# Optimization experiments

Measured on AMD Instinct MI355X. Metric: run time of the kernel, lower is better.

## Reference

```python
import jax, jax.numpy as jnp
import numpy as np

H = 4      # heads
DK = 64    # d // heads
EPS = 1e-5 # LayerNorm eps

def setup_inputs() -> dict:
    key = jax.random.key(0)
    ks = jax.random.split(key, 8)
    N, NC, D = 16384, 32, 256
    s = 0.02
    return {
        'parent_vec': jax.random.normal(ks[0], (N, D), jnp.float32),
        'child_vecs': jax.random.normal(ks[1], (N, NC, D), jnp.float32),
        'child_idx': jax.random.randint(ks[2], (N, NC), 0, NC, jnp.int64),
        'Wq': jax.random.normal(ks[3], (D, D), jnp.float32) * s,
        'Wkv': jax.random.normal(ks[4], (2 * D, D), jnp.float32) * s,
        'pos_emb': jax.random.normal(ks[5], (NC, D), jnp.float32) * s,
        'Wout': jax.random.normal(ks[6], (D, D), jnp.float32) * s,
        'bout': jnp.zeros((D,), jnp.float32),
        'ln_gamma': jnp.ones((D,), jnp.float32),
        'ln_beta': jnp.zeros((D,), jnp.float32),
    }

def reference(parent_vec, child_vecs, child_idx, Wq, Wkv, pos_emb, Wout, bout, ln_gamma, ln_beta):
    N, NC, D = child_vecs.shape
    # add position embedding to each child (gather)
    kv_in = child_vecs + pos_emb[child_idx]                     # [N, NC, D]
    kv = jnp.einsum('bnd,ed->bne', kv_in, Wkv)                  # [N, NC, 2D]
    k, v = jnp.split(kv, 2, axis=-1)
    k = k.reshape(N, NC, H, DK)
    v = v.reshape(N, NC, H, DK)
    q = (parent_vec @ Wq.T).reshape(N, H, DK)                   # [N, H, DK]
    scores = jnp.einsum('bnhd,bhd->bnh', k, q) * (DK ** -0.5)   # [N, NC, H]
    att = jax.nn.softmax(scores, axis=1)                        # over children
    ctx = jnp.einsum('bnh,bnhd->bhd', att, v).reshape(N, D)     # [N, D]
    out = ctx @ Wout.T + bout                                   # dropout: eval mode (identity)
    x = parent_vec + out
    mu = jnp.mean(x, axis=-1, keepdims=True)
    var = jnp.var(x, axis=-1, keepdims=True)
    return (x - mu) * jax.lax.rsqrt(var + EPS) * ln_gamma + ln_beta
```

## Files before the change

### kernel.cpp

```cpp
#include <hip/hip_runtime.h>
#include <hip/hip_bf16.h>
#include <string.h>

typedef __attribute__((ext_vector_type(8))) short short8;
typedef __attribute__((ext_vector_type(4))) float f32x4;

#define D_DIM 256
#define NC_DIM 32
#define KV_PAD 260

__device__ __forceinline__ ushort f2bf(float x) {
    union { float f; unsigned u; } v; v.f = x;
    unsigned r = (v.u + 0x7fffu + ((v.u >> 16) & 1u)) >> 16;
    return (ushort)r;
}
__device__ __forceinline__ float bf2f(ushort u) {
    union { unsigned u32; float f; } v; v.u32 = ((unsigned)u) << 16;
    return v.f;
}

__global__ __launch_bounds__(256)
void k_combine_B(const float* __restrict__ Wq, const float* __restrict__ Wkv,
                 ushort* __restrict__ Bc2t) {
    int bid = blockIdx.x;
    int h = bid >> 8, d = bid & 255;
    int i = threadIdx.x;
    __shared__ float wk_s[64];
    if (i < 64) wk_s[i] = Wkv[(size_t)(h * 64 + i) * D_DIM + d];
    __syncthreads();
    float s = 0.f;
#pragma unroll 8
    for (int j = 0; j < 64; j++)
        s = fmaf(Wq[(size_t)(h * 64 + j) * D_DIM + i], wk_s[j], s);
    Bc2t[(size_t)(h * 256 + d) * D_DIM + i] = f2bf(s);
}

__global__ __launch_bounds__(256)
void k_combine_C(const float* __restrict__ Wkv, const float* __restrict__ Wout,
                 ushort* __restrict__ Cc2t) {
    int bid = blockIdx.x;
    int h = bid >> 8, i = bid & 255;
    int d = threadIdx.x;
    __shared__ float wo_s[64];
    if (d < 64) wo_s[d] = Wout[(size_t)i * D_DIM + h * 64 + d];
    __syncthreads();
    const float* Wv = Wkv + 256 * D_DIM;
    float s = 0.f;
#pragma unroll 8
    for (int dk = 0; dk < 64; dk++)
        s = fmaf(Wv[(size_t)(h * 64 + dk) * D_DIM + d], wo_s[dk], s);
    Cc2t[(size_t)i * 1024 + h * 256 + d] = f2bf(s);
}

template <bool A_F32, bool EPI_RES>
__global__ __launch_bounds__(256)
void k_gemm(const void* __restrict__ Ap, const ushort* __restrict__ Bt,
            void* __restrict__ Cp, const float* __restrict__ resid,
            const float* __restrict__ bias, int M, int N, int K) {
    __shared__ ushort As[64][40];
    __shared__ ushort Bs[64][40];
    const int tid = threadIdx.x;
    const int m0 = blockIdx.y * 64, n0 = blockIdx.x * 64;
    const int w = tid >> 6, L = tid & 63;
    const int ar = tid >> 2, ac = (tid & 3) * 8;
    f32x4 acc0 = {0.f, 0.f, 0.f, 0.f}, acc1 = {0.f, 0.f, 0.f, 0.f};
    f32x4 acc2 = {0.f, 0.f, 0.f, 0.f}, acc3 = {0.f, 0.f, 0.f, 0.f};

    for (int k0 = 0; k0 < K; k0 += 32) {
        __syncthreads();
        if (A_F32) {
            const float* A = (const float*)Ap;
            const float* src = A + (size_t)(m0 + ar) * K + k0 + ac;
            float4 v0 = *(const float4*)src;
            float4 v1 = *(const float4*)(src + 4);
            union { ushort us[8]; uint4 v; } pk;
            pk.us[0] = f2bf(v0.x); pk.us[1] = f2bf(v0.y);
            pk.us[2] = f2bf(v0.z); pk.us[3] = f2bf(v0.w);
            pk.us[4] = f2bf(v1.x); pk.us[5] = f2bf(v1.y);
            pk.us[6] = f2bf(v1.z); pk.us[7] = f2bf(v1.w);
            *(uint4*)&As[ar][ac] = pk.v;
        } else {
            const ushort* A = (const ushort*)Ap;
            *(uint4*)&As[ar][ac] = *(const uint4*)(A + (size_t)(m0 + ar) * K + k0 + ac);
        }
        *(uint4*)&Bs[ar][ac] = *(const uint4*)(Bt + (size_t)(n0 + ar) * K + k0 + ac);
        __syncthreads();
        short8 af = *(const short8*)&As[w * 16 + (L & 15)][(L >> 4) * 8];
        short8 b0 = *(const short8*)&Bs[0 + (L & 15)][(L >> 4) * 8];
        short8 b1 = *(const short8*)&Bs[16 + (L & 15)][(L >> 4) * 8];
        short8 b2 = *(const short8*)&Bs[32 + (L & 15)][(L >> 4) * 8];
        short8 b3 = *(const short8*)&Bs[48 + (L & 15)][(L >> 4) * 8];
        acc0 = __builtin_amdgcn_mfma_f32_16x16x32_bf16(af, b0, acc0, 0, 0, 0);
        acc1 = __builtin_amdgcn_mfma_f32_16x16x32_bf16(af, b1, acc1, 0, 0, 0);
        acc2 = __builtin_amdgcn_mfma_f32_16x16x32_bf16(af, b2, acc2, 0, 0, 0);
        acc3 = __builtin_amdgcn_mfma_f32_16x16x32_bf16(af, b3, acc3, 0, 0, 0);
    }
    const int row_base = m0 + w * 16 + (L >> 4) * 4;
    const int col_base = n0 + (L & 15);
    f32x4 accs[4] = {acc0, acc1, acc2, acc3};
#pragma unroll
    for (int nt = 0; nt < 4; nt++) {
        int col = col_base + nt * 16;
#pragma unroll
        for (int r = 0; r < 4; r++) {
            int row = row_base + r;
            float v = accs[nt][r];
            if (EPI_RES) {
                ((float*)Cp)[(size_t)row * N + col] =
                    v + resid[(size_t)row * N + col] + bias[col];
            } else {
                ((ushort*)Cp)[(size_t)row * N + col] = f2bf(v);
            }
        }
    }
}

__global__ __launch_bounds__(256)
void k_attn(const float* __restrict__ child, const int* __restrict__ idx,
            const float* __restrict__ pos_emb, ushort* __restrict__ Am) {
    __shared__ int idx_s[NC_DIM];
    __shared__ float A_s[4][KV_PAD];
    __shared__ float kv_s[NC_DIM][KV_PAD];
    __shared__ float part_s[8][NC_DIM][4];
    __shared__ float att_s[NC_DIM][4];
    __shared__ float mpart_s[4][4][D_DIM];
    const int b = blockIdx.x;
    const int t = threadIdx.x;

    if (t < NC_DIM) idx_s[t] = idx[(size_t)b * NC_DIM + t];
    if (t < 128) {
        uint4 raw = *(const uint4*)(Am + (size_t)b * 1024 + t * 8);
        const ushort* u = (const ushort*)&raw;
        int h = t >> 5, c = (t & 31) * 8;
#pragma unroll
        for (int j = 0; j < 8; j++) A_s[h][c + j] = bf2f(u[j]);
    }
    __syncthreads();

    const float4* ch4 = (const float4*)(child + (size_t)b * NC_DIM * D_DIM);
#pragma unroll
    for (int i = 0; i < 8; i++) {
        int f = t + i * 256;
        int n = f >> 6, c4 = f & 63;
        float4 cv = ch4[f];
        float4 pv = ((const float4*)(pos_emb + (size_t)idx_s[n] * D_DIM))[c4];
        float4 r;
        r.x = cv.x + pv.x; r.y = cv.y + pv.y; r.z = cv.z + pv.z; r.w = cv.w + pv.w;
        *(float4*)&kv_s[n][c4 * 4] = r;
    }
    __syncthreads();

    {
        int n = t & 31, c = t >> 5;
        float s0 = 0, s1 = 0, s2 = 0, s3 = 0;
#pragma unroll
        for (int j = 0; j < 32; j += 4) {
            float4 kv = *(const float4*)&kv_s[n][c * 32 + j];
            float4 a0 = *(const float4*)&A_s[0][c * 32 + j];
            float4 a1 = *(const float4*)&A_s[1][c * 32 + j];
            float4 a2 = *(const float4*)&A_s[2][c * 32 + j];
            float4 a3 = *(const float4*)&A_s[3][c * 32 + j];
            s0 += kv.x * a0.x + kv.y * a0.y + kv.z * a0.z + kv.w * a0.w;
            s1 += kv.x * a1.x + kv.y * a1.y + kv.z * a1.z + kv.w * a1.w;
            s2 += kv.x * a2.x + kv.y * a2.y + kv.z * a2.z + kv.w * a2.w;
            s3 += kv.x * a3.x + kv.y * a3.y + kv.z * a3.z + kv.w * a3.w;
        }
        part_s[c][n][0] = s0; part_s[c][n][1] = s1;
        part_s[c][n][2] = s2; part_s[c][n][3] = s3;
    }
    __syncthreads();

    if (t < 128) {
        int n = t & 31, h = t >> 5;
        float s = 0;
#pragma unroll
        for (int c = 0; c < 8; c++) s += part_s[c][n][h];
        s *= 0.125f;
        float mx = s;
#pragma unroll
        for (int off = 16; off; off >>= 1) mx = fmaxf(mx, __shfl_xor(mx, off, 32));
        float e = __expf(s - mx);
        float sum = e;
#pragma unroll
        for (int off = 16; off; off >>= 1) sum += __shfl_xor(sum, off, 32);
        att_s[n][h] = e / sum;
    }
    __syncthreads();

    {
        int d4 = t & 63, g = t >> 6;
        float4 a0 = {0, 0, 0, 0}, a1 = {0, 0, 0, 0}, a2 = {0, 0, 0, 0}, a3 = {0, 0, 0, 0};
#pragma unroll
        for (int nn = 0; nn < 8; nn++) {
            int n = g * 8 + nn;
            float4 kv = *(const float4*)&kv_s[n][d4 * 4];
            float w0 = att_s[n][0], w1 = att_s[n][1], w2 = att_s[n][2], w3 = att_s[n][3];
            a0.x += w0 * kv.x; a0.y += w0 * kv.y; a0.z += w0 * kv.z; a0.w += w0 * kv.w;
            a1.x += w1 * kv.x; a1.y += w1 * kv.y; a1.z += w1 * kv.z; a1.w += w1 * kv.w;
            a2.x += w2 * kv.x; a2.y += w2 * kv.y; a2.z += w2 * kv.z; a2.w += w2 * kv.w;
            a3.x += w3 * kv.x; a3.y += w3 * kv.y; a3.z += w3 * kv.z; a3.w += w3 * kv.w;
        }
        *(float4*)&mpart_s[g][0][d4 * 4] = a0;
        *(float4*)&mpart_s[g][1][d4 * 4] = a1;
        *(float4*)&mpart_s[g][2][d4 * 4] = a2;
        *(float4*)&mpart_s[g][3][d4 * 4] = a3;
    }
    __syncthreads();

    {
        int h = t >> 6, d4 = t & 63;
        float4 m = {0, 0, 0, 0};
#pragma unroll
        for (int g = 0; g < 4; g++) {
            float4 p = *(const float4*)&mpart_s[g][h][d4 * 4];
            m.x += p.x; m.y += p.y; m.z += p.z; m.w += p.w;
        }
        union { ushort us[4]; uint2 v; } pk;
        pk.us[0] = f2bf(m.x); pk.us[1] = f2bf(m.y);
        pk.us[2] = f2bf(m.z); pk.us[3] = f2bf(m.w);
        *(uint2*)(Am + (size_t)b * 1024 + h * 256 + d4 * 4) = pk.v;
    }
}

__global__ __launch_bounds__(256)
void k_ln(const float* __restrict__ x, const float* __restrict__ gamma,
          const float* __restrict__ beta, float* __restrict__ out) {
    const int t = threadIdx.x;
    const int w = t >> 6, l = t & 63;
    const size_t row = (size_t)blockIdx.x * 4 + w;
    float4 v = *(const float4*)(x + row * D_DIM + l * 4);
    float s = v.x + v.y + v.z + v.w;
    float q = v.x * v.x + v.y * v.y + v.z * v.z + v.w * v.w;
#pragma unroll
    for (int off = 32; off; off >>= 1) {
        s += __shfl_xor(s, off, 64);
        q += __shfl_xor(q, off, 64);
    }
    float mu = s * (1.f / 256.f);
    float var = q * (1.f / 256.f) - mu * mu;
    float rs = rsqrtf(var + 1e-5f);
    float4 g4 = *(const float4*)(gamma + l * 4);
    float4 b4 = *(const float4*)(beta + l * 4);
    float4 o;
    o.x = (v.x - mu) * rs * g4.x + b4.x;
    o.y = (v.y - mu) * rs * g4.y + b4.y;
    o.z = (v.z - mu) * rs * g4.z + b4.z;
    o.w = (v.w - mu) * rs * g4.w + b4.w;
    *(float4*)(out + row * D_DIM + l * 4) = o;
}

extern "C" void kernel_launch(void* const* d_in, const int* in_sizes, int n_in,
                              void* d_out, int out_size, void* d_ws, size_t ws_size,
                              hipStream_t stream) {
    const float* parent = (const float*)d_in[0];
    const float* child  = (const float*)d_in[1];
    const int*   cidx   = (const int*)d_in[2];
    const float* Wq     = (const float*)d_in[3];
    const float* Wkv    = (const float*)d_in[4];
    const float* pos    = (const float*)d_in[5];
    const float* Wout   = (const float*)d_in[6];
    const float* bout   = (const float*)d_in[7];
    const float* gamma  = (const float*)d_in[8];
    const float* beta   = (const float*)d_in[9];
    const int N = in_sizes[0] / D_DIM;

    char* ws = (char*)d_ws;
    float*  x_ws = (float*)ws;
    ushort* Am   = (ushort*)(ws + (size_t)N * D_DIM * 4);
    ushort* Bc2t = (ushort*)(ws + (size_t)N * D_DIM * 4 + (size_t)N * 1024 * 2);
    ushort* Cc2t = Bc2t + 1024 * 256;

    k_combine_B<<<1024, 256, 0, stream>>>(Wq, Wkv, Bc2t);
    k_combine_C<<<1024, 256, 0, stream>>>(Wkv, Wout, Cc2t);
    k_gemm<true, false><<<dim3(1024 / 64, N / 64), 256, 0, stream>>>(
        parent, Bc2t, Am, nullptr, nullptr, N, 1024, 256);
    k_attn<<<N, 256, 0, stream>>>(child, cidx, pos, Am);
    k_gemm<false, true><<<dim3(256 / 64, N / 64), 256, 0, stream>>>(
        Am, Cc2t, x_ws, parent, bout, N, 256, 1024);
    k_ln<<<N / 4, 256, 0, stream>>>(x_ws, gamma, beta, (float*)d_out);
}
```

Measured before the change: 827.0 us.

## Enlarge GEMM tiles with direct-to-LDS loads, pre-convert parent, streamline attention

After: 788.2 us. -4.7%, faster.

```diff
diff --git a/kernel.cpp b/kernel.cpp
--- a/kernel.cpp
+++ b/kernel.cpp
@@ -1,6 +1,5 @@
 #include <hip/hip_runtime.h>
 #include <hip/hip_bf16.h>
-#include <string.h>
 
 typedef __attribute__((ext_vector_type(8))) short short8;
 typedef __attribute__((ext_vector_type(4))) float f32x4;
@@ -17,6 +16,22 @@
 __device__ __forceinline__ float bf2f(ushort u) {
     union { unsigned u32; float f; } v; v.u32 = ((unsigned)u) << 16;
     return v.f;
+}
+
+__device__ __forceinline__ void gload_lds16(const ushort* g, ushort* lds) {
+    __builtin_amdgcn_global_load_lds(
+        (const __attribute__((address_space(1))) unsigned int*)g,
+        (__attribute__((address_space(3))) unsigned int*)lds, 16, 0, 0);
+}
+
+__global__ __launch_bounds__(256)
+void k_cvt(const float4* __restrict__ src, uint4* __restrict__ dst) {
+    int j = blockIdx.x * 256 + threadIdx.x;
+    float4 a = src[2 * j], b = src[2 * j + 1];
+    union { ushort us[8]; uint4 v; } pk;
+    pk.us[0] = f2bf(a.x); pk.us[1] = f2bf(a.y); pk.us[2] = f2bf(a.z); pk.us[3] = f2bf(a.w);
+    pk.us[4] = f2bf(b.x); pk.us[5] = f2bf(b.y); pk.us[6] = f2bf(b.z); pk.us[7] = f2bf(b.w);
+    dst[j] = pk.v;
 }
 
 __global__ __launch_bounds__(256)
@@ -52,70 +67,68 @@
     Cc2t[(size_t)i * 1024 + h * 256 + d] = f2bf(s);
 }
 
-template <bool A_F32, bool EPI_RES>
-__global__ __launch_bounds__(256)
-void k_gemm(const void* __restrict__ Ap, const ushort* __restrict__ Bt,
+template <bool EPI_RES>
+__global__ __launch_bounds__(256, 2)
+void k_gemm(const ushort* __restrict__ A, const ushort* __restrict__ Bt,
             void* __restrict__ Cp, const float* __restrict__ resid,
             const float* __restrict__ bias, int M, int N, int K) {
-    __shared__ ushort As[64][40];
-    __shared__ ushort Bs[64][40];
+    __shared__ ushort As[128][64];
+    __shared__ ushort Bs[128][64];
     const int tid = threadIdx.x;
-    const int m0 = blockIdx.y * 64, n0 = blockIdx.x * 64;
-    const int w = tid >> 6, L = tid & 63;
-    const int ar = tid >> 2, ac = (tid & 3) * 8;
-    f32x4 acc0 = {0.f, 0.f, 0.f, 0.f}, acc1 = {0.f, 0.f, 0.f, 0.f};
-    f32x4 acc2 = {0.f, 0.f, 0.f, 0.f}, acc3 = {0.f, 0.f, 0.f, 0.f};
-
-    for (int k0 = 0; k0 < K; k0 += 32) {
+    const int w = tid >> 6, l = tid & 63;
+    const int m0 = blockIdx.y * 128, n0 = blockIdx.x * 128;
+    const int wr = (w >> 1) * 64, wc = (w & 1) * 64;
+    const int srow = l >> 3, scol = (l & 7) * 8;
+    f32x4 acc[4][4] = {};
+
+    for (int k0 = 0; k0 < K; k0 += 64) {
         __syncthreads();
-        if (A_F32) {
-            const float* A = (const float*)Ap;
-            const float* src = A + (size_t)(m0 + ar) * K + k0 + ac;
-            float4 v0 = *(const float4*)src;
-            float4 v1 = *(const float4*)(src + 4);
-            union { ushort us[8]; uint4 v; } pk;
-            pk.us[0] = f2bf(v0.x); pk.us[1] = f2bf(v0.y);
-            pk.us[2] = f2bf(v0.z); pk.us[3] = f2bf(v0.w);
-            pk.us[4] = f2bf(v1.x); pk.us[5] = f2bf(v1.y);
-            pk.us[6] = f2bf(v1.z); pk.us[7] = f2bf(v1.w);
-            *(uint4*)&As[ar][ac] = pk.v;
-        } else {
-            const ushort* A = (const ushort*)Ap;
-            *(uint4*)&As[ar][ac] = *(const uint4*)(A + (size_t)(m0 + ar) * K + k0 + ac);
-        }
-        *(uint4*)&Bs[ar][ac] = *(const uint4*)(Bt + (size_t)(n0 + ar) * K + k0 + ac);
+#pragma unroll
+        for (int j = 0; j < 4; j++) {
+            int c = w * 4 + j;
+            int r = c * 8 + srow;
+            gload_lds16(A  + (size_t)(m0 + r) * K + k0 + scol, &As[c * 8][0]);
+            gload_lds16(Bt + (size_t)(n0 + r) * K + k0 + scol, &Bs[c * 8][0]);
+        }
         __syncthreads();
-        short8 af = *(const short8*)&As[w * 16 + (L & 15)][(L >> 4) * 8];
-        short8 b0 = *(const short8*)&Bs[0 + (L & 15)][(L >> 4) * 8];
-        short8 b1 = *(const short8*)&Bs[16 + (L & 15)][(L >> 4) * 8];
-        short8 b2 = *(const short8*)&Bs[32 + (L & 15)][(L >> 4) * 8];
-        short8 b3 = *(const short8*)&Bs[48 + (L & 15)][(L >> 4) * 8];
-        acc0 = __builtin_amdgcn_mfma_f32_16x16x32_bf16(af, b0, acc0, 0, 0, 0);
-        acc1 = __builtin_amdgcn_mfma_f32_16x16x32_bf16(af, b1, acc1, 0, 0, 0);
-        acc2 = __builtin_amdgcn_mfma_f32_16x16x32_bf16(af, b2, acc2, 0, 0, 0);
-        acc3 = __builtin_amdgcn_mfma_f32_16x16x32_bf16(af, b3, acc3, 0, 0, 0);
-    }
-    const int row_base = m0 + w * 16 + (L >> 4) * 4;
-    const int col_base = n0 + (L & 15);
-    f32x4 accs[4] = {acc0, acc1, acc2, acc3};
-#pragma unroll
-    for (int nt = 0; nt < 4; nt++) {
-        int col = col_base + nt * 16;
-#pragma unroll
-        for (int r = 0; r < 4; r++) {
-            int row = row_base + r;
-            float v = accs[nt][r];
-            if (EPI_RES) {
-                ((float*)Cp)[(size_t)row * N + col] =
-                    v + resid[(size_t)row * N + col] + bias[col];
-            } else {
-                ((ushort*)Cp)[(size_t)row * N + col] = f2bf(v);
+#pragma unroll
+        for (int ks = 0; ks < 2; ks++) {
+            short8 af[4], bf[4];
+#pragma unroll
+            for (int i = 0; i < 4; i++)
+                af[i] = *(const short8*)&As[wr + i * 16 + (l & 15)][ks * 32 + (l >> 4) * 8];
+#pragma unroll
+            for (int i = 0; i < 4; i++)
+                bf[i] = *(const short8*)&Bs[wc + i * 16 + (l & 15)][ks * 32 + (l >> 4) * 8];
+#pragma unroll
+            for (int i = 0; i < 4; i++)
+#pragma unroll
+                for (int j = 0; j < 4; j++)
+                    acc[i][j] = __builtin_amdgcn_mfma_f32_16x16x32_bf16(af[i], bf[j], acc[i][j], 0, 0, 0);
+        }
+    }
+    const int row0 = m0 + wr + (l >> 4) * 4;
+    const int col0 = n0 + wc + (l & 15);
+#pragma unroll
+    for (int i = 0; i < 4; i++)
+#pragma unroll
+        for (int j = 0; j < 4; j++) {
+            int col = col0 + j * 16;
+#pragma unroll
+            for (int r = 0; r < 4; r++) {
+                int row = row0 + i * 16 + r;
+                float v = acc[i][j][r];
+                if (EPI_RES) {
+                    ((float*)Cp)[(size_t)row * N + col] =
+                        v + resid[(size_t)row * N + col] + bias[col];
+                } else {
+                    ((ushort*)Cp)[(size_t)row * N + col] = f2bf(v);
+                }
             }
         }
-    }
-}
-
-__global__ __launch_bounds__(256)
+}
+
+__global__ __launch_bounds__(256, 3)
 void k_attn(const float* __restrict__ child, const int* __restrict__ idx,
             const float* __restrict__ pos_emb, ushort* __restrict__ Am) {
     __shared__ int idx_s[NC_DIM];
@@ -123,9 +136,14 @@
     __shared__ float kv_s[NC_DIM][KV_PAD];
     __shared__ float part_s[8][NC_DIM][4];
     __shared__ float att_s[NC_DIM][4];
-    __shared__ float mpart_s[4][4][D_DIM];
     const int b = blockIdx.x;
     const int t = threadIdx.x;
+    const int l = t & 63;
+
+    const float4* ch4 = (const float4*)(child + (size_t)b * NC_DIM * D_DIM);
+    float4 cv[8];
+#pragma unroll
+    for (int i = 0; i < 8; i++) cv[i] = ch4[t + i * 256];
 
     if (t < NC_DIM) idx_s[t] = idx[(size_t)b * NC_DIM + t];
     if (t < 128) {
@@ -137,16 +155,14 @@
     }
     __syncthreads();
 
-    const float4* ch4 = (const float4*)(child + (size_t)b * NC_DIM * D_DIM);
 #pragma unroll
     for (int i = 0; i < 8; i++) {
-        int f = t + i * 256;
-        int n = f >> 6, c4 = f & 63;
-        float4 cv = ch4[f];
-        float4 pv = ((const float4*)(pos_emb + (size_t)idx_s[n] * D_DIM))[c4];
+        int n = (t >> 6) + i * 4;
+        float4 pv = ((const float4*)(pos_emb + (size_t)idx_s[n] * D_DIM))[l];
         float4 r;
-        r.x = cv.x + pv.x; r.y = cv.y + pv.y; r.z = cv.z + pv.z; r.w = cv.w + pv.w;
-        *(float4*)&kv_s[n][c4 * 4] = r;
+        r.x = cv[i].x + pv.x; r.y = cv[i].y + pv.y;
+        r.z = cv[i].z + pv.z; r.w = cv[i].w + pv.w;
+        *(float4*)&kv_s[n][l * 4] = r;
     }
     __syncthreads();
 
@@ -165,8 +181,7 @@
             s2 += kv.x * a2.x + kv.y * a2.y + kv.z * a2.z + kv.w * a2.w;
             s3 += kv.x * a3.x + kv.y * a3.y + kv.z * a3.z + kv.w * a3.w;
         }
-        part_s[c][n][0] = s0; part_s[c][n][1] = s1;
-        part_s[c][n][2] = s2; part_s[c][n][3] = s3;
+        *(float4*)&part_s[c][n][0] = make_float4(s0, s1, s2, s3);
     }
     __syncthreads();
 
@@ -188,37 +203,19 @@
     __syncthreads();
 
     {
-        int d4 = t & 63, g = t >> 6;
-        float4 a0 = {0, 0, 0, 0}, a1 = {0, 0, 0, 0}, a2 = {0, 0, 0, 0}, a3 = {0, 0, 0, 0};
-#pragma unroll
-        for (int nn = 0; nn < 8; nn++) {
-            int n = g * 8 + nn;
-            float4 kv = *(const float4*)&kv_s[n][d4 * 4];
-            float w0 = att_s[n][0], w1 = att_s[n][1], w2 = att_s[n][2], w3 = att_s[n][3];
-            a0.x += w0 * kv.x; a0.y += w0 * kv.y; a0.z += w0 * kv.z; a0.w += w0 * kv.w;
-            a1.x += w1 * kv.x; a1.y += w1 * kv.y; a1.z += w1 * kv.z; a1.w += w1 * kv.w;
-            a2.x += w2 * kv.x; a2.y += w2 * kv.y; a2.z += w2 * kv.z; a2.w += w2 * kv.w;
-            a3.x += w3 * kv.x; a3.y += w3 * kv.y; a3.z += w3 * kv.z; a3.w += w3 * kv.w;
-        }
-        *(float4*)&mpart_s[g][0][d4 * 4] = a0;
-        *(float4*)&mpart_s[g][1][d4 * 4] = a1;
-        *(float4*)&mpart_s[g][2][d4 * 4] = a2;
-        *(float4*)&mpart_s[g][3][d4 * 4] = a3;
-    }
-    __syncthreads();
-
-    {
-        int h = t >> 6, d4 = t & 63;
-        float4 m = {0, 0, 0, 0};
-#pragma unroll
-        for (int g = 0; g < 4; g++) {
-            float4 p = *(const float4*)&mpart_s[g][h][d4 * 4];
-            m.x += p.x; m.y += p.y; m.z += p.z; m.w += p.w;
+        int h = t >> 6;
+        float4 m = {0.f, 0.f, 0.f, 0.f};
+#pragma unroll
+        for (int n = 0; n < NC_DIM; n++) {
+            float wgt = att_s[n][h];
+            float4 kv = *(const float4*)&kv_s[n][l * 4];
+            m.x += wgt * kv.x; m.y += wgt * kv.y;
+            m.z += wgt * kv.z; m.w += wgt * kv.w;
         }
         union { ushort us[4]; uint2 v; } pk;
         pk.us[0] = f2bf(m.x); pk.us[1] = f2bf(m.y);
         pk.us[2] = f2bf(m.z); pk.us[3] = f2bf(m.w);
-        *(uint2*)(Am + (size_t)b * 1024 + h * 256 + d4 * 4) = pk.v;
+        *(uint2*)(Am + (size_t)b * 1024 + h * 256 + l * 4) = pk.v;
     }
 }
 
@@ -265,17 +262,21 @@
     const int N = in_sizes[0] / D_DIM;
 
     char* ws = (char*)d_ws;
-    float*  x_ws = (float*)ws;
-    ushort* Am   = (ushort*)(ws + (size_t)N * D_DIM * 4);
-    ushort* Bc2t = (ushort*)(ws + (size_t)N * D_DIM * 4 + (size_t)N * 1024 * 2);
-    ushort* Cc2t = Bc2t + 1024 * 256;
-
+    size_t off = 0;
+    float*  x_ws = (float*)(ws + off);  off += (size_t)N * D_DIM * 4;
+    ushort* Am   = (ushort*)(ws + off); off += (size_t)N * 1024 * 2;
+    ushort* pbf  = (ushort*)(ws + off); off += (size_t)N * D_DIM * 2;
+    ushort* Bc2t = (ushort*)(ws + off); off += (size_t)1024 * 256 * 2;
+    ushort* Cc2t = (ushort*)(ws + off);
+
+    k_cvt<<<(N * D_DIM / 8 + 255) / 256, 256, 0, stream>>>(
+        (const float4*)parent, (uint4*)pbf);
     k_combine_B<<<1024, 256, 0, stream>>>(Wq, Wkv, Bc2t);
     k_combine_C<<<1024, 256, 0, stream>>>(Wkv, Wout, Cc2t);
-    k_gemm<true, false><<<dim3(1024 / 64, N / 64), 256, 0, stream>>>(
-        parent, Bc2t, Am, nullptr, nullptr, N, 1024, 256);
+    k_gemm<false><<<dim3(1024 / 128, N / 128), 256, 0, stream>>>(
+        pbf, Bc2t, Am, nullptr, nullptr, N, 1024, 256);
     k_attn<<<N, 256, 0, stream>>>(child, cidx, pos, Am);
-    k_gemm<false, true><<<dim3(256 / 64, N / 64), 256, 0, stream>>>(
+    k_gemm<true><<<dim3(256 / 128, N / 128), 256, 0, stream>>>(
         Am, Cc2t, x_ws, parent, bout, N, 256, 1024);
     k_ln<<<N / 4, 256, 0, stream>>>(x_ws, gamma, beta, (float*)d_out);
 }
```
